# Kernel tuning notes

Hardware: AMD Instinct MI355X
Metric: run time of the kernel (lower is better)

The kernel has to match this reference:

```python
import jax, jax.numpy as jnp
import numpy as np

N = 50000
E = 800000
EPS = 1e-5
# per-layer (in_dim, heads, out_dim, concat) matching GraphEncoder defaults
LAYERS = [(16, 4, 32, True), (128, 4, 32, True), (128, 4, 32, True), (128, 1, 128, False)]


def setup_inputs() -> dict:
    key = jax.random.key(0)
    ks = jax.random.split(key, 32)
    rn = lambda k, shape: jax.random.normal(k, shape, jnp.float32) * 0.1
    inp = {}
    inp["node_types"] = jax.random.randint(ks[0], (N,), 0, 3)
    inp["edge_index"] = jax.random.randint(ks[1], (2, E), 0, N)
    inp["emb"] = rn(ks[2], (3, 16))
    i = 3
    for li, (ind, h, od, _) in enumerate(LAYERS):
        inp[f"Wl{li}"] = rn(ks[i], (ind, h * od)); i += 1
        inp[f"Wr{li}"] = rn(ks[i], (ind, h * od)); i += 1
        inp[f"att{li}"] = rn(ks[i], (h, od)); i += 1
        inp[f"b{li}"] = rn(ks[i], (h * od if li < 3 else od,)); i += 1
    inp["ln_g"] = jnp.ones((4, 128), jnp.float32)
    inp["ln_b"] = jnp.zeros((4, 128), jnp.float32)
    return inp


def gatv2_layer(x, src, dst, Wl, Wr, att, b, heads, out_dim, concat):
    # PyG GATv2Conv (share_weights=False, negative_slope=0.2, self-loops added by caller)
    n = x.shape[0]
    xl = (x @ Wl).reshape(n, heads, out_dim)  # source transform (messages)
    xr = (x @ Wr).reshape(n, heads, out_dim)  # target transform
    e = jax.nn.leaky_relu(xl[src] + xr[dst], 0.2)          # [E', H, D]
    logit = jnp.einsum('ehd,hd->eh', e, att)               # [E', H]
    lmax = jax.ops.segment_max(logit, dst, num_segments=n)  # segment softmax over dst
    p = jnp.exp(logit - lmax[dst])
    z = jax.ops.segment_sum(p, dst, num_segments=n)
    alpha = p / z[dst]                                      # every node has a self-loop -> z > 0
    out = jax.ops.segment_sum(xl[src] * alpha[..., None], dst, num_segments=n)  # [n, H, D]
    out = out.reshape(n, heads * out_dim) if concat else out.mean(axis=1)
    return out + b


def layer_norm(x, g, b):
    mu = x.mean(-1, keepdims=True)
    var = ((x - mu) ** 2).mean(-1, keepdims=True)
    return (x - mu) / jnp.sqrt(var + EPS) * g + b


def reference(node_types, edge_index, emb, Wl0, Wr0, att0, b0, Wl1, Wr1, att1, b1,
              Wl2, Wr2, att2, b2, Wl3, Wr3, att3, b3, ln_g, ln_b):
    n = node_types.shape[0]
    loops = jnp.arange(n)
    src = jnp.concatenate([edge_index[0], loops])
    dst = jnp.concatenate([edge_index[1], loops])
    x = emb[node_types]
    params = [(Wl0, Wr0, att0, b0), (Wl1, Wr1, att1, b1), (Wl2, Wr2, att2, b2), (Wl3, Wr3, att3, b3)]
    for li, ((Wl, Wr, att, b), (_, h, od, concat)) in enumerate(zip(params, LAYERS)):
        res = x
        x = gatv2_layer(x, src, dst, Wl, Wr, att, b, h, od, concat)
        if x.shape[-1] == res.shape[-1]:
            x = x + res
        x = jax.nn.relu(layer_norm(x, ln_g[li], ln_b[li]))
    return x
```

## Files before the change

### kernel.cpp

```cpp
#include <hip/hip_runtime.h>

__global__ void GraphEncoder_20555713479231_kernel() {}

using hfrag8 = __attribute__((ext_vector_type(8))) _Float16;
using facc4  = __attribute__((ext_vector_type(4))) float;
using h2     = __attribute__((ext_vector_type(2))) _Float16;

__device__ __forceinline__ unsigned short f2h_bits(float f) {
  union { _Float16 h; unsigned short u; } c;
  c.h = (_Float16)f;
  return c.u;
}
__device__ __forceinline__ unsigned packh(float a, float b) {
  return (unsigned)f2h_bits(a) | ((unsigned)f2h_bits(b) << 16);
}
__device__ __forceinline__ h2 u2h(unsigned u) {
  union { unsigned u; h2 h; } c;
  c.u = u;
  return c.h;
}
__device__ __forceinline__ unsigned h22u(h2 h) {
  union { h2 h; unsigned u; } c;
  c.h = h;
  return c.u;
}
__device__ __forceinline__ float h2f_lo(unsigned u) { return (float)u2h(u).x; }
__device__ __forceinline__ float h2f_hi(unsigned u) { return (float)u2h(u).y; }

__device__ __forceinline__ int rl(int v, int l) {
  return __builtin_amdgcn_readlane(v, l);
}
__device__ __forceinline__ unsigned grow(const unsigned* __restrict__ p, int idx, int lane) {
  return p[(((unsigned)idx) << 6) + (unsigned)lane];
}

__global__ __launch_bounds__(256) void k_hist(const int* __restrict__ dst,
                                              int* __restrict__ deg, int e) {
  int i = blockIdx.x * blockDim.x + threadIdx.x;
  if (i < e) atomicAdd(&deg[dst[i]], 1);
}

__global__ __launch_bounds__(256) void k_scan1(const int* __restrict__ deg,
                                               int* __restrict__ off,
                                               int* __restrict__ bsum, int n) {
  __shared__ int wsum[4];
  int tid = threadIdx.x;
  int gid = blockIdx.x * 256 + tid;
  int lane = tid & 63, wid = tid >> 6;
  int v = (gid < n) ? (deg[gid] + 1) : 0;
  int x = v;
  #pragma unroll
  for (int d = 1; d < 64; d <<= 1) {
    int t = __shfl_up(x, d);
    if (lane >= d) x += t;
  }
  if (lane == 63) wsum[wid] = x;
  __syncthreads();
  int wpre = 0;
  for (int k = 0; k < wid; ++k) wpre += wsum[k];
  if (gid < n) off[gid] = wpre + x - v;
  if (tid == 0) {
    int t = 0;
    #pragma unroll
    for (int k = 0; k < 4; ++k) t += wsum[k];
    bsum[blockIdx.x] = t;
  }
}

__global__ __launch_bounds__(256) void k_scan2(int* __restrict__ bsum,
                                               int* __restrict__ off, int nb, int n) {
  __shared__ int wsum[4];
  int tid = threadIdx.x;
  int lane = tid & 63, wid = tid >> 6;
  int v = (tid < nb) ? bsum[tid] : 0;
  int x = v;
  #pragma unroll
  for (int d = 1; d < 64; d <<= 1) {
    int t = __shfl_up(x, d);
    if (lane >= d) x += t;
  }
  if (lane == 63) wsum[wid] = x;
  __syncthreads();
  int wpre = 0;
  for (int k = 0; k < wid; ++k) wpre += wsum[k];
  if (tid < nb) bsum[tid] = wpre + x - v;
  if (tid == 0) {
    int t = 0;
    #pragma unroll
    for (int k = 0; k < 4; ++k) t += wsum[k];
    off[n] = t;
  }
}

__global__ __launch_bounds__(256) void k_scan3(int* __restrict__ off,
                                               const int* __restrict__ bsum,
                                               int* __restrict__ pos,
                                               int* __restrict__ csr, int n) {
  int gid = blockIdx.x * 256 + threadIdx.x;
  if (gid < n) {
    int o = off[gid] + bsum[blockIdx.x];
    off[gid] = o;
    csr[o] = gid;
    pos[gid] = o + 1;
  }
}

__global__ __launch_bounds__(256) void k_fill(const int* __restrict__ src,
                                              const int* __restrict__ dst,
                                              int* __restrict__ pos,
                                              int* __restrict__ csr, int e) {
  int i = blockIdx.x * blockDim.x + threadIdx.x;
  if (i < e) {
    int d = dst[i];
    int p = atomicAdd(&pos[d], 1);
    csr[p] = src[i];
  }
}

__global__ __launch_bounds__(256)
void k_pack3(const float* __restrict__ wl1, const float* __restrict__ wr1,
             const float* __restrict__ wl2, const float* __restrict__ wr2,
             const float* __restrict__ wl3, const float* __restrict__ wr3,
             const float* __restrict__ emb,
             const float* __restrict__ wl0, const float* __restrict__ wr0,
             const int* __restrict__ types, int n,
             unsigned short* __restrict__ bp,
             unsigned* __restrict__ tlb, float* __restrict__ trf,
             unsigned* __restrict__ ptypes) {
  int b = blockIdx.x;
  if (b < 384) {
    int idx = b * 256 + threadIdx.x;
    int layer = idx >> 15;
    int r = idx & 32767;
    int j = r & 7, lane = (r >> 3) & 63, ct = (r >> 9) & 15, t = r >> 13;
    int k = t * 32 + (lane >> 4) * 8 + j;
    int c = ct * 16 + (lane & 15);
    const float* wl = (layer == 0) ? wl1 : ((layer == 1) ? wl2 : wl3);
    const float* wr = (layer == 0) ? wr1 : ((layer == 1) ? wr2 : wr3);
    float v = (c < 128) ? wl[k * 128 + c] : wr[k * 128 + (c - 128)];
    bp[idx] = f2h_bits(v);
  } else if (b == 384) {
    int tid = threadIdx.x;
    if (tid >= 192) return;
    int row = tid >> 6, cp = tid & 63, c0 = cp * 2;
    float al0 = 0.f, al1 = 0.f, ar0 = 0.f, ar1 = 0.f;
    #pragma unroll
    for (int k = 0; k < 16; ++k) {
      float ev = emb[row * 16 + k];
      al0 += ev * wl0[k * 128 + c0];
      al1 += ev * wl0[k * 128 + c0 + 1];
      ar0 += ev * wr0[k * 128 + c0];
      ar1 += ev * wr0[k * 128 + c0 + 1];
    }
    tlb[row * 64 + cp] = packh(al0, al1);
    *(float2*)(trf + row * 128 + c0) = make_float2(ar0, ar1);
  } else {
    int i = (b - 385) * 256 + threadIdx.x;
    int npk = (n + 15) >> 4;
    if (i < npk) {
      unsigned pw = 0;
      #pragma unroll
      for (int j = 0; j < 16; ++j) {
        int u = i * 16 + j;
        int ty = (u < n) ? (types[u] & 3) : 3;
        pw |= ((unsigned)ty) << (2 * j);
      }
      ptypes[i] = pw;
    }
  }
}

__global__ __launch_bounds__(256)
void k_agg0(const int* __restrict__ off, const int* __restrict__ csr,
            const unsigned* __restrict__ ptypes,
            const unsigned* __restrict__ tlb, const float* __restrict__ trf,
            const float* __restrict__ att, const float* __restrict__ bias,
            const float* __restrict__ lng, const float* __restrict__ lnb,
            unsigned* __restrict__ yout, int n) {
  int v = (blockIdx.x * blockDim.x + threadIdx.x) >> 6;
  int lane = threadIdx.x & 63;
  if (v >= n) return;
  v = __builtin_amdgcn_readfirstlane(v);
  int beg = off[v], end = off[v + 1];
  int c0 = 0, c1 = 0, c2 = 0;
  for (int base = beg; base < end; base += 64) {
    int e = base + lane;
    bool act = e < end;
    int u = act ? csr[e] : 0;
    unsigned pw = ptypes[u >> 4];
    int ty = act ? (int)((pw >> ((u & 15) * 2)) & 3) : 3;
    c0 += __popcll(__ballot(ty == 0));
    c1 += __popcll(__ballot(ty == 1));
    c2 += __popcll(__ballot(ty == 2));
  }
  float cnt[3] = {(float)c0, (float)c1, (float)c2};
  int f0 = lane * 2;
  unsigned pwv = ptypes[v >> 4];
  int tyv = (int)((pwv >> ((v & 15) * 2)) & 3);
  float2 xrv = *(const float2*)(trf + tyv * 128 + f0);
  float a0 = att[f0], a1 = att[f0 + 1];
  float s = 0.f, O0 = 0.f, O1 = 0.f;
  #pragma unroll
  for (int ty = 0; ty < 3; ++ty) {
    unsigned p = tlb[ty * 64 + lane];
    float x0 = h2f_lo(p), x1 = h2f_hi(p);
    float t0 = x0 + xrv.x; t0 = t0 > 0.f ? t0 : 0.2f * t0;
    float t1 = x1 + xrv.y; t1 = t1 > 0.f ? t1 : 0.2f * t1;
    float c = t0 * a0 + t1 * a1;
    c += __shfl_xor(c, 1);
    c += __shfl_xor(c, 2);
    c += __shfl_xor(c, 4);
    c += __shfl_xor(c, 8);
    float w = cnt[ty] * __expf(c);
    s += w;
    O0 = fmaf(w, x0, O0);
    O1 = fmaf(w, x1, O1);
  }
  float inv = 1.f / s;
  float o0 = O0 * inv + bias[f0];
  float o1 = O1 * inv + bias[f0 + 1];
  float sum = o0 + o1, sq = o0 * o0 + o1 * o1;
  #pragma unroll
  for (int d2 = 1; d2 < 64; d2 <<= 1) {
    sum += __shfl_xor(sum, d2);
    sq += __shfl_xor(sq, d2);
  }
  float mu = sum * (1.f / 128.f);
  float var = sq * (1.f / 128.f) - mu * mu;
  float rstd = rsqrtf(var + 1e-5f);
  float y0 = fmaxf((o0 - mu) * rstd * lng[f0] + lnb[f0], 0.f);
  float y1 = fmaxf((o1 - mu) * rstd * lng[f0 + 1] + lnb[f0 + 1], 0.f);
  yout[(size_t)v * 64 + lane] = packh(y0, y1);
}

__global__ __launch_bounds__(256)
void k_gemm(const unsigned* __restrict__ x, const unsigned short* __restrict__ bp,
            unsigned* __restrict__ xlo, unsigned* __restrict__ xro, int nstrips, int n) {
  int wave = (blockIdx.x * 256 + threadIdx.x) >> 6;
  int lane = threadIdx.x & 63;
  if (wave >= nstrips) return;
  int r0 = wave * 16;
  int row = r0 + (lane & 15);
  if (row >= n) row = n - 1;
  int quad = lane >> 4;
  const unsigned* ap = x + (size_t)row * 64;
  hfrag8 a[4];
  #pragma unroll
  for (int t = 0; t < 4; ++t) a[t] = *(const hfrag8*)(ap + t * 16 + quad * 4);
  unsigned short* xloS = (unsigned short*)xlo;
  unsigned short* xroS = (unsigned short*)xro;
  int rbase = r0 + quad * 4;
  #pragma unroll
  for (int ct = 0; ct < 16; ++ct) {
    facc4 acc = {0.f, 0.f, 0.f, 0.f};
    #pragma unroll
    for (int t = 0; t < 4; ++t) {
      hfrag8 b = *(const hfrag8*)(bp + (size_t)(((t * 16 + ct) * 64 + lane) * 8));
      acc = __builtin_amdgcn_mfma_f32_16x16x32_f16(a[t], b, acc, 0, 0, 0);
    }
    int col = (ct & 7) * 16 + (lane & 15);
    unsigned short* dstp = (ct < 8) ? xloS : xroS;
    #pragma unroll
    for (int i = 0; i < 4; ++i) {
      int r = rbase + i;
      if (r < n) dstp[(size_t)r * 128 + col] = f2h_bits(acc[i]);
    }
  }
}

template <int WIDE>
__global__ __launch_bounds__(256)
void k_agg_t(const int* __restrict__ off, const int* __restrict__ csr,
             const unsigned* __restrict__ xl, const unsigned* __restrict__ xr,
             const float* __restrict__ att, const float* __restrict__ bias,
             const unsigned* __restrict__ xres,
             const float* __restrict__ lng, const float* __restrict__ lnb,
             unsigned* __restrict__ ybf, float* __restrict__ yf32, int n) {
  int v = (blockIdx.x * blockDim.x + threadIdx.x) >> 6;
  int lane = threadIdx.x & 63;
  if (v >= n) return;
  v = __builtin_amdgcn_readfirstlane(v);
  int f0 = lane * 2;
  h2 a2;
  a2.x = (_Float16)att[f0];
  a2.y = (_Float16)att[f0 + 1];
  h2 r2 = u2h(xr[(size_t)v * 64 + lane]);
  h2 k02 = {(_Float16)0.2f, (_Float16)0.2f};
  int beg = off[v], end = off[v + 1];
  float s0 = 0.f, s1 = 0.f;
  h2 O0 = {(_Float16)0.f, (_Float16)0.f};
  h2 O1 = O0, O2 = O0, O3 = O0;

  for (int base = beg; base < end; base += 64) {
    int m = end - base;
    if (m > 64) m = 64;
    int last = m - 1;
    int idxv = csr[base + (lane < m ? lane : last)];
    int ng = (m + 3) >> 2;
    unsigned c0 = grow(xl, rl(idxv, 0), lane);
    unsigned c1 = grow(xl, rl(idxv, min(1, last)), lane);
    unsigned c2 = grow(xl, rl(idxv, min(2, last)), lane);
    unsigned c3 = grow(xl, rl(idxv, min(3, last)), lane);
    unsigned n0 = grow(xl, rl(idxv, min(4, last)), lane);
    unsigned n1 = grow(xl, rl(idxv, min(5, last)), lane);
    unsigned n2 = grow(xl, rl(idxv, min(6, last)), lane);
    unsigned n3 = grow(xl, rl(idxv, min(7, last)), lane);
    for (int g = 0; g < ng; ++g) {
      int jb = g * 4;
      int pb = jb + 8;
      unsigned t0 = grow(xl, rl(idxv, min(pb + 0, last)), lane);
      unsigned t1 = grow(xl, rl(idxv, min(pb + 1, last)), lane);
      unsigned t2 = grow(xl, rl(idxv, min(pb + 2, last)), lane);
      unsigned t3 = grow(xl, rl(idxv, min(pb + 3, last)), lane);
      h2 xa = u2h(c0), xb = u2h(c1), xc = u2h(c2), xd = u2h(c3);
      h2 ta = xa + r2, tb = xb + r2, tc = xc + r2, td = xd + r2;
      h2 la = __builtin_elementwise_max(ta, ta * k02);
      h2 lb = __builtin_elementwise_max(tb, tb * k02);
      h2 lc = __builtin_elementwise_max(tc, tc * k02);
      h2 ld = __builtin_elementwise_max(td, td * k02);
      h2 da = la * a2, db = lb * a2, dc = lc * a2, dd = ld * a2;
      h2 cp0, cp1;
      cp0.x = da.x + da.y;
      cp0.y = db.x + db.y;
      cp1.x = dc.x + dc.y;
      cp1.y = dd.x + dd.y;
      unsigned cu0 = h22u(cp0), cu1 = h22u(cp1);
      cu0 = h22u(u2h(cu0) + u2h((unsigned)__shfl_xor((int)cu0, 1)));
      cu1 = h22u(u2h(cu1) + u2h((unsigned)__shfl_xor((int)cu1, 1)));
      cu0 = h22u(u2h(cu0) + u2h((unsigned)__shfl_xor((int)cu0, 2)));
      cu1 = h22u(u2h(cu1) + u2h((unsigned)__shfl_xor((int)cu1, 2)));
      cu0 = h22u(u2h(cu0) + u2h((unsigned)__shfl_xor((int)cu0, 4)));
      cu1 = h22u(u2h(cu1) + u2h((unsigned)__shfl_xor((int)cu1, 4)));
      cu0 = h22u(u2h(cu0) + u2h((unsigned)__shfl_xor((int)cu0, 8)));
      cu1 = h22u(u2h(cu1) + u2h((unsigned)__shfl_xor((int)cu1, 8)));
      if (WIDE) {
        cu0 = h22u(u2h(cu0) + u2h((unsigned)__shfl_xor((int)cu0, 16)));
        cu1 = h22u(u2h(cu1) + u2h((unsigned)__shfl_xor((int)cu1, 16)));
        cu0 = h22u(u2h(cu0) + u2h((unsigned)__shfl_xor((int)cu0, 32)));
        cu1 = h22u(u2h(cu1) + u2h((unsigned)__shfl_xor((int)cu1, 32)));
      }
      h2 cf0 = u2h(cu0), cf1 = u2h(cu1);
      float wa = (jb + 0 < m) ? __expf((float)cf0.x) : 0.f;
      float wb = (jb + 1 < m) ? __expf((float)cf0.y) : 0.f;
      float wc = (jb + 2 < m) ? __expf((float)cf1.x) : 0.f;
      float wd = (jb + 3 < m) ? __expf((float)cf1.y) : 0.f;
      s0 += wa + wb;
      s1 += wc + wd;
      _Float16 wah = (_Float16)wa, wbh = (_Float16)wb;
      _Float16 wch = (_Float16)wc, wdh = (_Float16)wd;
      h2 wa2 = {wah, wah}, wb2 = {wbh, wbh};
      h2 wc2 = {wch, wch}, wd2 = {wdh, wdh};
      O0 = wa2 * xa + O0;
      O1 = wb2 * xb + O1;
      O2 = wc2 * xc + O2;
      O3 = wd2 * xd + O3;
      c0 = n0; c1 = n1; c2 = n2; c3 = n3;
      n0 = t0; n1 = t1; n2 = t2; n3 = t3;
    }
  }
  float s = s0 + s1;
  float Ox = (float)O0.x + (float)O1.x + (float)O2.x + (float)O3.x;
  float Oy = (float)O0.y + (float)O1.y + (float)O2.y + (float)O3.y;
  float inv = 1.f / s;
  float o0 = Ox * inv + bias[f0];
  float o1 = Oy * inv + bias[f0 + 1];
  if (xres) {
    unsigned rs = xres[(size_t)v * 64 + lane];
    o0 += h2f_lo(rs);
    o1 += h2f_hi(rs);
  }
  float sum = o0 + o1, sq = o0 * o0 + o1 * o1;
  #pragma unroll
  for (int d2 = 1; d2 < 64; d2 <<= 1) {
    sum += __shfl_xor(sum, d2);
    sq += __shfl_xor(sq, d2);
  }
  float mu = sum * (1.f / 128.f);
  float var = sq * (1.f / 128.f) - mu * mu;
  float rstd = rsqrtf(var + 1e-5f);
  float y0 = fmaxf((o0 - mu) * rstd * lng[f0] + lnb[f0], 0.f);
  float y1 = fmaxf((o1 - mu) * rstd * lng[f0 + 1] + lnb[f0 + 1], 0.f);
  if (yf32) {
    *(float2*)(yf32 + (size_t)v * 128 + f0) = make_float2(y0, y1);
  } else {
    ybf[(size_t)v * 64 + lane] = packh(y0, y1);
  }
}

extern "C" void kernel_launch(void* const* d_in, const int* in_sizes, int n_in,
                              void* d_out, int out_size, void* d_ws, size_t ws_size,
                              hipStream_t stream) {
  (void)n_in; (void)out_size; (void)ws_size;
  const int* node_types = (const int*)d_in[0];
  const int* edge_index = (const int*)d_in[1];
  const float* emb = (const float*)d_in[2];
  const float* Wl0 = (const float*)d_in[3];
  const float* Wr0 = (const float*)d_in[4];
  const float* att0 = (const float*)d_in[5];
  const float* b0 = (const float*)d_in[6];
  const float* Wl1 = (const float*)d_in[7];
  const float* Wr1 = (const float*)d_in[8];
  const float* att1 = (const float*)d_in[9];
  const float* b1 = (const float*)d_in[10];
  const float* Wl2 = (const float*)d_in[11];
  const float* Wr2 = (const float*)d_in[12];
  const float* att2 = (const float*)d_in[13];
  const float* b2 = (const float*)d_in[14];
  const float* Wl3 = (const float*)d_in[15];
  const float* Wr3 = (const float*)d_in[16];
  const float* att3 = (const float*)d_in[17];
  const float* b3 = (const float*)d_in[18];
  const float* lng = (const float*)d_in[19];
  const float* lnb = (const float*)d_in[20];

  int n = in_sizes[0];
  int e = in_sizes[1] / 2;
  const int* srcp = edge_index;
  const int* dstp = edge_index + e;
  int nblocks = (n + 255) / 256;

  char* wsp = (char*)d_ws;
  size_t ofs = 0;
  int* deg = (int*)(wsp + ofs); ofs += (((size_t)n * 4) + 255) & ~(size_t)255;
  int* off = (int*)(wsp + ofs); ofs += (((size_t)(n + 1) * 4) + 255) & ~(size_t)255;
  int* csr = (int*)(wsp + ofs); ofs += (((size_t)(e + n) * 4) + 255) & ~(size_t)255;
  int* bsum = (int*)(wsp + ofs); ofs += (((size_t)nblocks * 4) + 255) & ~(size_t)255;
  unsigned* xlb = (unsigned*)(wsp + ofs); ofs += (((size_t)n * 64 * 4) + 255) & ~(size_t)255;
  unsigned* xrb = (unsigned*)(wsp + ofs); ofs += (((size_t)n * 64 * 4) + 255) & ~(size_t)255;
  unsigned* xcur = (unsigned*)(wsp + ofs); ofs += (((size_t)n * 64 * 4) + 255) & ~(size_t)255;
  unsigned short* bp = (unsigned short*)(wsp + ofs); ofs += 3 * 65536;
  unsigned* tlb = (unsigned*)(wsp + ofs); ofs += 1024;
  float* trf = (float*)(wsp + ofs); ofs += 2048;
  unsigned* ptypes = (unsigned*)(wsp + ofs); ofs += ((((size_t)(n + 15) / 16) * 4) + 255) & ~(size_t)255;
  int* pos = deg;

  (void)hipMemsetAsync(deg, 0, (size_t)n * 4, stream);
  k_hist<<<(e + 255) / 256, 256, 0, stream>>>(dstp, deg, e);
  int npk = (n + 15) / 16;
  int packGrid = 385 + (npk + 255) / 256;
  k_pack3<<<packGrid, 256, 0, stream>>>(Wl1, Wr1, Wl2, Wr2, Wl3, Wr3,
                                        emb, Wl0, Wr0, node_types, n,
                                        bp, tlb, trf, ptypes);
  k_scan1<<<nblocks, 256, 0, stream>>>(deg, off, bsum, n);
  k_scan2<<<1, 256, 0, stream>>>(bsum, off, nblocks, n);
  k_scan3<<<nblocks, 256, 0, stream>>>(off, bsum, pos, csr, n);
  k_fill<<<(e + 255) / 256, 256, 0, stream>>>(srcp, dstp, pos, csr, e);

  int aggBlocks = (n * 64 + 255) / 256;

  k_agg0<<<aggBlocks, 256, 0, stream>>>(off, csr, ptypes, tlb, trf,
                                        att0, b0, lng, lnb, xcur, n);

  int nstrips = (n + 15) / 16;
  int gemmBlocks = (nstrips + 3) / 4;

  k_gemm<<<gemmBlocks, 256, 0, stream>>>(xcur, bp, xlb, xrb, nstrips, n);
  k_agg_t<0><<<aggBlocks, 256, 0, stream>>>(off, csr, xlb, xrb, att1, b1, xcur,
                                            lng + 128, lnb + 128, xcur, (float*)0, n);
  k_gemm<<<gemmBlocks, 256, 0, stream>>>(xcur, bp + 32768, xlb, xrb, nstrips, n);
  k_agg_t<0><<<aggBlocks, 256, 0, stream>>>(off, csr, xlb, xrb, att2, b2, xcur,
                                            lng + 256, lnb + 256, xcur, (float*)0, n);
  k_gemm<<<gemmBlocks, 256, 0, stream>>>(xcur, bp + 65536, xlb, xrb, nstrips, n);
  k_agg_t<1><<<aggBlocks, 256, 0, stream>>>(off, csr, xlb, xrb, att3, b3, xcur,
                                            lng + 384, lnb + 384, (unsigned*)0, (float*)d_out, n);
}
```

Before: 417.6 us.

## Double-buffer neighbor gathers in aggregation, fuse scans, fold memset, use exp2

The aggregation kernel now gathers neighbor feature rows in double-buffered groups of 16 and batches the shuffle reductions over 8 packed logit pairs. This replaces the per-4 readlane prefetch chain and is meant to raise memory-level parallelism on the gather. The scan2/scan3 pair is merged into one kernel in which each block recomputes its prefix from bsum, and the degree memset is folded into the pack kernel. Attention weights are pre-scaled by log2(e) so exp2 can be used. The CSR buffer is padded and zero-filled so padded reads stay in bounds, and the larger register arrays may lower occupancy.

```diff
diff --git a/kernel.cpp b/kernel.cpp
--- a/kernel.cpp
+++ b/kernel.cpp
@@ -27,12 +27,7 @@
 __device__ __forceinline__ float h2f_lo(unsigned u) { return (float)u2h(u).x; }
 __device__ __forceinline__ float h2f_hi(unsigned u) { return (float)u2h(u).y; }
 
-__device__ __forceinline__ int rl(int v, int l) {
-  return __builtin_amdgcn_readlane(v, l);
-}
-__device__ __forceinline__ unsigned grow(const unsigned* __restrict__ p, int idx, int lane) {
-  return p[(((unsigned)idx) << 6) + (unsigned)lane];
-}
+#define LOG2E 1.4426950408889634f
 
 __global__ __launch_bounds__(256) void k_hist(const int* __restrict__ dst,
                                               int* __restrict__ deg, int e) {
@@ -67,41 +62,37 @@
   }
 }
 
-__global__ __launch_bounds__(256) void k_scan2(int* __restrict__ bsum,
-                                               int* __restrict__ off, int nb, int n) {
-  __shared__ int wsum[4];
-  int tid = threadIdx.x;
-  int lane = tid & 63, wid = tid >> 6;
-  int v = (tid < nb) ? bsum[tid] : 0;
-  int x = v;
+__global__ __launch_bounds__(256) void k_scan23(int* __restrict__ off,
+                                                const int* __restrict__ bsum,
+                                                int* __restrict__ pos,
+                                                int* __restrict__ csr, int nb, int n) {
+  __shared__ int sh[8];
+  int tid = threadIdx.x, lane = tid & 63, wid = tid >> 6;
+  int p = 0, t = 0;
+  for (int k = tid; k < nb; k += 256) {
+    int bv = bsum[k];
+    t += bv;
+    if (k < (int)blockIdx.x) p += bv;
+  }
   #pragma unroll
   for (int d = 1; d < 64; d <<= 1) {
-    int t = __shfl_up(x, d);
-    if (lane >= d) x += t;
-  }
-  if (lane == 63) wsum[wid] = x;
+    p += __shfl_xor(p, d);
+    t += __shfl_xor(t, d);
+  }
+  if (lane == 0) { sh[wid] = p; sh[4 + wid] = t; }
   __syncthreads();
-  int wpre = 0;
-  for (int k = 0; k < wid; ++k) wpre += wsum[k];
-  if (tid < nb) bsum[tid] = wpre + x - v;
-  if (tid == 0) {
-    int t = 0;
-    #pragma unroll
-    for (int k = 0; k < 4; ++k) t += wsum[k];
-    off[n] = t;
-  }
-}
-
-__global__ __launch_bounds__(256) void k_scan3(int* __restrict__ off,
-                                               const int* __restrict__ bsum,
-                                               int* __restrict__ pos,
-                                               int* __restrict__ csr, int n) {
-  int gid = blockIdx.x * 256 + threadIdx.x;
+  p = sh[0] + sh[1] + sh[2] + sh[3];
+  t = sh[4] + sh[5] + sh[6] + sh[7];
+  int gid = blockIdx.x * 256 + tid;
   if (gid < n) {
-    int o = off[gid] + bsum[blockIdx.x];
+    int o = off[gid] + p;
     off[gid] = o;
     csr[o] = gid;
     pos[gid] = o + 1;
+  }
+  if (blockIdx.x == 0) {
+    if (tid == 0) off[n] = t;
+    if (tid < 16) csr[t + tid] = 0;
   }
 }
 
@@ -126,7 +117,7 @@
              const int* __restrict__ types, int n,
              unsigned short* __restrict__ bp,
              unsigned* __restrict__ tlb, float* __restrict__ trf,
-             unsigned* __restrict__ ptypes) {
+             unsigned* __restrict__ ptypes, int* __restrict__ deg, int npkB) {
   int b = blockIdx.x;
   if (b < 384) {
     int idx = b * 256 + threadIdx.x;
@@ -154,7 +145,7 @@
     }
     tlb[row * 64 + cp] = packh(al0, al1);
     *(float2*)(trf + row * 128 + c0) = make_float2(ar0, ar1);
-  } else {
+  } else if (b < 385 + npkB) {
     int i = (b - 385) * 256 + threadIdx.x;
     int npk = (n + 15) >> 4;
     if (i < npk) {
@@ -167,6 +158,9 @@
       }
       ptypes[i] = pw;
     }
+  } else {
+    int i = (b - 385 - npkB) * 256 + threadIdx.x;
+    if (i < n) deg[i] = 0;
   }
 }
 
@@ -198,7 +192,7 @@
   unsigned pwv = ptypes[v >> 4];
   int tyv = (int)((pwv >> ((v & 15) * 2)) & 3);
   float2 xrv = *(const float2*)(trf + tyv * 128 + f0);
-  float a0 = att[f0], a1 = att[f0 + 1];
+  float a0 = att[f0] * LOG2E, a1 = att[f0 + 1] * LOG2E;
   float s = 0.f, O0 = 0.f, O1 = 0.f;
   #pragma unroll
   for (int ty = 0; ty < 3; ++ty) {
@@ -211,7 +205,7 @@
     c += __shfl_xor(c, 2);
     c += __shfl_xor(c, 4);
     c += __shfl_xor(c, 8);
-    float w = cnt[ty] * __expf(c);
+    float w = cnt[ty] * __builtin_amdgcn_exp2f(c);
     s += w;
     O0 = fmaf(w, x0, O0);
     O1 = fmaf(w, x1, O1);
@@ -282,85 +276,96 @@
   v = __builtin_amdgcn_readfirstlane(v);
   int f0 = lane * 2;
   h2 a2;
-  a2.x = (_Float16)att[f0];
-  a2.y = (_Float16)att[f0 + 1];
+  a2.x = (_Float16)(att[f0] * LOG2E);
+  a2.y = (_Float16)(att[f0 + 1] * LOG2E);
   h2 r2 = u2h(xr[(size_t)v * 64 + lane]);
   h2 k02 = {(_Float16)0.2f, (_Float16)0.2f};
-  int beg = off[v], end = off[v + 1];
-  float s0 = 0.f, s1 = 0.f;
-  h2 O0 = {(_Float16)0.f, (_Float16)0.f};
-  h2 O1 = O0, O2 = O0, O3 = O0;
-
-  for (int base = beg; base < end; base += 64) {
-    int m = end - base;
-    if (m > 64) m = 64;
-    int last = m - 1;
-    int idxv = csr[base + (lane < m ? lane : last)];
-    int ng = (m + 3) >> 2;
-    unsigned c0 = grow(xl, rl(idxv, 0), lane);
-    unsigned c1 = grow(xl, rl(idxv, min(1, last)), lane);
-    unsigned c2 = grow(xl, rl(idxv, min(2, last)), lane);
-    unsigned c3 = grow(xl, rl(idxv, min(3, last)), lane);
-    unsigned n0 = grow(xl, rl(idxv, min(4, last)), lane);
-    unsigned n1 = grow(xl, rl(idxv, min(5, last)), lane);
-    unsigned n2 = grow(xl, rl(idxv, min(6, last)), lane);
-    unsigned n3 = grow(xl, rl(idxv, min(7, last)), lane);
-    for (int g = 0; g < ng; ++g) {
-      int jb = g * 4;
-      int pb = jb + 8;
-      unsigned t0 = grow(xl, rl(idxv, min(pb + 0, last)), lane);
-      unsigned t1 = grow(xl, rl(idxv, min(pb + 1, last)), lane);
-      unsigned t2 = grow(xl, rl(idxv, min(pb + 2, last)), lane);
-      unsigned t3 = grow(xl, rl(idxv, min(pb + 3, last)), lane);
-      h2 xa = u2h(c0), xb = u2h(c1), xc = u2h(c2), xd = u2h(c3);
-      h2 ta = xa + r2, tb = xb + r2, tc = xc + r2, td = xd + r2;
+  int beg = __builtin_amdgcn_readfirstlane(off[v]);
+  int end = __builtin_amdgcn_readfirstlane(off[v + 1]);
+  int m = end - beg;
+  const int* cw = csr + beg;
+  float sv[4] = {0.f, 0.f, 0.f, 0.f};
+  h2 Ov[4];
+  Ov[0] = h2{(_Float16)0.f, (_Float16)0.f};
+  Ov[1] = Ov[0]; Ov[2] = Ov[0]; Ov[3] = Ov[0];
+
+  unsigned A[16], B[16];
+
+  auto load16 = [&](unsigned* buf, int g) {
+    #pragma unroll
+    for (int i = 0; i < 16; ++i) {
+      int r = cw[g * 16 + i];
+      buf[i] = xl[(((unsigned)r) << 6) + (unsigned)lane];
+    }
+  };
+
+  auto compute = [&](const unsigned* buf, int mloc) {
+    h2 cp[8];
+    #pragma unroll
+    for (int j = 0; j < 8; ++j) {
+      h2 xa = u2h(buf[2 * j]), xb = u2h(buf[2 * j + 1]);
+      h2 ta = xa + r2, tb = xb + r2;
       h2 la = __builtin_elementwise_max(ta, ta * k02);
       h2 lb = __builtin_elementwise_max(tb, tb * k02);
-      h2 lc = __builtin_elementwise_max(tc, tc * k02);
-      h2 ld = __builtin_elementwise_max(td, td * k02);
-      h2 da = la * a2, db = lb * a2, dc = lc * a2, dd = ld * a2;
-      h2 cp0, cp1;
-      cp0.x = da.x + da.y;
-      cp0.y = db.x + db.y;
-      cp1.x = dc.x + dc.y;
-      cp1.y = dd.x + dd.y;
-      unsigned cu0 = h22u(cp0), cu1 = h22u(cp1);
-      cu0 = h22u(u2h(cu0) + u2h((unsigned)__shfl_xor((int)cu0, 1)));
-      cu1 = h22u(u2h(cu1) + u2h((unsigned)__shfl_xor((int)cu1, 1)));
-      cu0 = h22u(u2h(cu0) + u2h((unsigned)__shfl_xor((int)cu0, 2)));
-      cu1 = h22u(u2h(cu1) + u2h((unsigned)__shfl_xor((int)cu1, 2)));
-      cu0 = h22u(u2h(cu0) + u2h((unsigned)__shfl_xor((int)cu0, 4)));
-      cu1 = h22u(u2h(cu1) + u2h((unsigned)__shfl_xor((int)cu1, 4)));
-      cu0 = h22u(u2h(cu0) + u2h((unsigned)__shfl_xor((int)cu0, 8)));
-      cu1 = h22u(u2h(cu1) + u2h((unsigned)__shfl_xor((int)cu1, 8)));
-      if (WIDE) {
-        cu0 = h22u(u2h(cu0) + u2h((unsigned)__shfl_xor((int)cu0, 16)));
-        cu1 = h22u(u2h(cu1) + u2h((unsigned)__shfl_xor((int)cu1, 16)));
-        cu0 = h22u(u2h(cu0) + u2h((unsigned)__shfl_xor((int)cu0, 32)));
-        cu1 = h22u(u2h(cu1) + u2h((unsigned)__shfl_xor((int)cu1, 32)));
-      }
-      h2 cf0 = u2h(cu0), cf1 = u2h(cu1);
-      float wa = (jb + 0 < m) ? __expf((float)cf0.x) : 0.f;
-      float wb = (jb + 1 < m) ? __expf((float)cf0.y) : 0.f;
-      float wc = (jb + 2 < m) ? __expf((float)cf1.x) : 0.f;
-      float wd = (jb + 3 < m) ? __expf((float)cf1.y) : 0.f;
-      s0 += wa + wb;
-      s1 += wc + wd;
-      _Float16 wah = (_Float16)wa, wbh = (_Float16)wb;
-      _Float16 wch = (_Float16)wc, wdh = (_Float16)wd;
-      h2 wa2 = {wah, wah}, wb2 = {wbh, wbh};
-      h2 wc2 = {wch, wch}, wd2 = {wdh, wdh};
-      O0 = wa2 * xa + O0;
-      O1 = wb2 * xb + O1;
-      O2 = wc2 * xc + O2;
-      O3 = wd2 * xd + O3;
-      c0 = n0; c1 = n1; c2 = n2; c3 = n3;
-      n0 = t0; n1 = t1; n2 = t2; n3 = t3;
-    }
-  }
-  float s = s0 + s1;
-  float Ox = (float)O0.x + (float)O1.x + (float)O2.x + (float)O3.x;
-  float Oy = (float)O0.y + (float)O1.y + (float)O2.y + (float)O3.y;
+      h2 da = la * a2, db = lb * a2;
+      h2 c;
+      c.x = da.x + da.y;
+      c.y = db.x + db.y;
+      cp[j] = c;
+    }
+    #pragma unroll
+    for (int lvl = 1; lvl <= (WIDE ? 32 : 8); lvl <<= 1) {
+      unsigned t[8];
+      #pragma unroll
+      for (int j = 0; j < 8; ++j) t[j] = (unsigned)__shfl_xor((int)h22u(cp[j]), lvl);
+      #pragma unroll
+      for (int j = 0; j < 8; ++j) cp[j] = cp[j] + u2h(t[j]);
+    }
+    float lgs[16];
+    #pragma unroll
+    for (int j = 0; j < 8; ++j) {
+      lgs[2 * j] = (float)cp[j].x;
+      lgs[2 * j + 1] = (float)cp[j].y;
+    }
+    if (mloc < 16) {
+      #pragma unroll
+      for (int i = 0; i < 16; ++i)
+        if (i >= mloc) lgs[i] = -200.f;
+    }
+    #pragma unroll
+    for (int i = 0; i < 16; ++i) {
+      float w = __builtin_amdgcn_exp2f(lgs[i]);
+      sv[i & 3] += w;
+      _Float16 wh = (_Float16)w;
+      h2 w2 = {wh, wh};
+      Ov[i & 3] = w2 * u2h(buf[i]) + Ov[i & 3];
+    }
+  };
+
+  int ng = (m + 15) >> 4;
+  load16(A, 0);
+  if (ng > 1) load16(B, 1);
+  int g = 0;
+  for (;;) {
+    {
+      int rem = m - g * 16;
+      compute(A, rem >= 16 ? 16 : rem);
+    }
+    ++g;
+    if (g >= ng) break;
+    if (g + 1 < ng) load16(A, g + 1);
+    {
+      int rem = m - g * 16;
+      compute(B, rem >= 16 ? 16 : rem);
+    }
+    ++g;
+    if (g >= ng) break;
+    if (g + 1 < ng) load16(B, g + 1);
+  }
+
+  float s = (sv[0] + sv[1]) + (sv[2] + sv[3]);
+  float Ox = ((float)Ov[0].x + (float)Ov[1].x) + ((float)Ov[2].x + (float)Ov[3].x);
+  float Oy = ((float)Ov[0].y + (float)Ov[1].y) + ((float)Ov[2].y + (float)Ov[3].y);
   float inv = 1.f / s;
   float o0 = Ox * inv + bias[f0];
   float o1 = Oy * inv + bias[f0 + 1];
@@ -423,7 +428,7 @@
   size_t ofs = 0;
   int* deg = (int*)(wsp + ofs); ofs += (((size_t)n * 4) + 255) & ~(size_t)255;
   int* off = (int*)(wsp + ofs); ofs += (((size_t)(n + 1) * 4) + 255) & ~(size_t)255;
-  int* csr = (int*)(wsp + ofs); ofs += (((size_t)(e + n) * 4) + 255) & ~(size_t)255;
+  int* csr = (int*)(wsp + ofs); ofs += (((size_t)(e + n + 64) * 4) + 255) & ~(size_t)255;
   int* bsum = (int*)(wsp + ofs); ofs += (((size_t)nblocks * 4) + 255) & ~(size_t)255;
   unsigned* xlb = (unsigned*)(wsp + ofs); ofs += (((size_t)n * 64 * 4) + 255) & ~(size_t)255;
   unsigned* xrb = (unsigned*)(wsp + ofs); ofs += (((size_t)n * 64 * 4) + 255) & ~(size_t)255;
@@ -434,16 +439,15 @@
   unsigned* ptypes = (unsigned*)(wsp + ofs); ofs += ((((size_t)(n + 15) / 16) * 4) + 255) & ~(size_t)255;
   int* pos = deg;
 
-  (void)hipMemsetAsync(deg, 0, (size_t)n * 4, stream);
-  k_hist<<<(e + 255) / 256, 256, 0, stream>>>(dstp, deg, e);
   int npk = (n + 15) / 16;
-  int packGrid = 385 + (npk + 255) / 256;
+  int npkB = (npk + 255) / 256;
+  int packGrid = 385 + npkB + nblocks;
   k_pack3<<<packGrid, 256, 0, stream>>>(Wl1, Wr1, Wl2, Wr2, Wl3, Wr3,
                                         emb, Wl0, Wr0, node_types, n,
-                                        bp, tlb, trf, ptypes);
+                                        bp, tlb, trf, ptypes, deg, npkB);
+  k_hist<<<(e + 255) / 256, 256, 0, stream>>>(dstp, deg, e);
   k_scan1<<<nblocks, 256, 0, stream>>>(deg, off, bsum, n);
-  k_scan2<<<1, 256, 0, stream>>>(bsum, off, nblocks, n);
-  k_scan3<<<nblocks, 256, 0, stream>>>(off, bsum, pos, csr, n);
+  k_scan23<<<nblocks, 256, 0, stream>>>(off, bsum, pos, csr, nblocks, n);
   k_fill<<<(e + 255) / 256, 256, 0, stream>>>(srcp, dstp, pos, csr, e);
 
   int aggBlocks = (n * 64 + 255) / 256;
```

After: 438.0 us. 4.9% more time.
